# Optimization experiments

Measured on AMD Instinct MI355X. Metric: run time of the kernel, lower is better.

The kernel has to match this reference:

```python
import jax, jax.numpy as jnp
import numpy as np

B = 256        # batch size
D = 256        # feature dim
N = 100000     # memory bank size (num pseudo classes)
TEMP = 0.07    # SCT_Memory temperature


def setup_inputs() -> dict:
    key = jax.random.key(0)
    k1, k2, k3 = jax.random.split(key, 3)
    inputs = jax.random.normal(k1, (B, D), dtype=jnp.float32)
    # ReID features are L2-normalized before hitting the memory
    inputs = inputs / jnp.linalg.norm(inputs, axis=1, keepdims=True)
    indexes = jax.random.randint(k2, (B,), 0, N, dtype=jnp.int32)
    features = jax.random.normal(k3, (N, D), dtype=jnp.float32)
    features = features / jnp.linalg.norm(features, axis=1, keepdims=True)
    return {"inputs": inputs, "indexes": indexes, "features": features,
            "momentum": 0.2}


def reference(inputs, indexes, features, momentum):
    # ExemplarMemory.forward: outputs = inputs.mm(features.t())
    # SCT_Memory then scales by 1/temp to form cluster_score.
    out = jnp.matmul(inputs, features.T)  # [B, N]
    return out / TEMP
```

## Files before the change

### kernel.cpp

```cpp
#include <hip/hip_runtime.h>
#include <hip/hip_bf16.h>


typedef __attribute__((ext_vector_type(8))) __bf16 bf16x8;
typedef __attribute__((ext_vector_type(4))) float  floatx4;
typedef __attribute__((ext_vector_type(4))) unsigned int uint4v;

#define NB 100000
#define KD 256
#define BN 128
#define NTILES 782
#define GRID 256
#define NCHUNK 32

union FragCast { uint4v u; bf16x8 f; };

__device__ __forceinline__ unsigned pk(float a, float b) {
  __hip_bfloat162 h = __float22bfloat162_rn(float2{a, b});
  union { __hip_bfloat162 h2; unsigned u; } c; c.h2 = h; return c.u;
}

__device__ __forceinline__ void barrier_lgkm() {
  asm volatile("s_waitcnt lgkmcnt(0)" ::: "memory");
  __builtin_amdgcn_s_barrier();
  asm volatile("" ::: "memory");
}

__global__ __launch_bounds__(1024, 4)
void sct_gemm(const float* __restrict__ inputs,
              const float* __restrict__ features,
              float* __restrict__ out) {
  __shared__ uint4v lds[BN][NCHUNK];

  const int tid  = threadIdx.x;
  const int ws   = tid >> 6;
  const int lane = tid & 63;
  const int quad = lane >> 4;
  const int l16  = lane & 15;
  const int q4   = quad * 4;
  const int e3   = l16 & 7;

  const int b = blockIdx.x;
  const int ntiles = (NTILES - b + GRID - 1) / GRID;

  const int srow = tid >> 3, sk = tid & 7;
  const int rswz = srow & 7;

  float4 pf[8];
  {
    const int n0 = b * BN;
    #pragma unroll
    for (int j = 0; j < 8; ++j) pf[j] = make_float4(0.f, 0.f, 0.f, 0.f);
    if (n0 + srow < NB) {
      const float4* p = (const float4*)(features + (size_t)(n0 + srow) * KD + sk * 32);
      #pragma unroll
      for (int j = 0; j < 8; ++j) pf[j] = p[j];
    }
  }

  const float scale = 1.0f / 0.07f;
  bf16x8 afrag[8];
  {
    const float* arow = inputs + (ws * 16 + l16) * KD + quad * 8;
    #pragma unroll
    for (int t = 0; t < 8; ++t) {
      const float4* p = (const float4*)(arow + t * 32);
      const float4 a0 = p[0], a1 = p[1];
      FragCast fc;
      fc.u.x = pk(a0.x * scale, a0.y * scale);
      fc.u.y = pk(a0.z * scale, a0.w * scale);
      fc.u.z = pk(a1.x * scale, a1.y * scale);
      fc.u.w = pk(a1.z * scale, a1.w * scale);
      afrag[t] = fc.f;
    }
  }

  float* const orow = out + (size_t)(ws * 16 + l16) * NB;

  for (int it = 0; it < ntiles; ++it) {
    const int n0 = (b + it * GRID) * BN;

    barrier_lgkm();

    {
      #pragma unroll
      for (int j = 0; j < 4; ++j) {
        uint4v w;
        w.x = pk(pf[2 * j].x, pf[2 * j].y);
        w.y = pk(pf[2 * j].z, pf[2 * j].w);
        w.z = pk(pf[2 * j + 1].x, pf[2 * j + 1].y);
        w.w = pk(pf[2 * j + 1].z, pf[2 * j + 1].w);
        lds[srow][(sk * 4 + j) ^ rswz] = w;
      }
    }

    barrier_lgkm();

    if (it + 1 < ntiles) {
      const int nn0 = (b + (it + 1) * GRID) * BN;
      #pragma unroll
      for (int j = 0; j < 8; ++j) pf[j] = make_float4(0.f, 0.f, 0.f, 0.f);
      if (nn0 + srow < NB) {
        const float4* p = (const float4*)(features + (size_t)(nn0 + srow) * KD + sk * 32);
        #pragma unroll
        for (int j = 0; j < 8; ++j) pf[j] = p[j];
      }
    }

    floatx4 acc[8];
    #pragma unroll
    for (int nt = 0; nt < 8; ++nt) acc[nt] = floatx4{0.f, 0.f, 0.f, 0.f};

    #pragma unroll
    for (int t = 0; t < 8; ++t) {
      #pragma unroll
      for (int nt = 0; nt < 8; ++nt) {
        FragCast fc;
        fc.u = lds[nt * 16 + l16][(t * 4 + quad) ^ e3];
        acc[nt] = __builtin_amdgcn_mfma_f32_16x16x32_bf16(fc.f, afrag[t], acc[nt], 0, 0, 0);
      }
    }

    #pragma unroll
    for (int nt = 0; nt < 8; ++nt) {
      const int n = n0 + nt * 16 + q4;
      if (n < NB)
        *(floatx4*)(orow + n) = acc[nt];
    }
  }
}

extern "C" void kernel_launch(void* const* d_in, const int* in_sizes, int n_in,
                              void* d_out, int out_size, void* d_ws, size_t ws_size,
                              hipStream_t stream) {
  const float* inputs   = (const float*)d_in[0];
  const float* features = (const float*)d_in[2];
  float* out = (float*)d_out;

  sct_gemm<<<GRID, 1024, 0, stream>>>(inputs, features, out);
}
```

Baseline: 214.2 us.

## Split batch across blocks with smaller N tiles and more, smaller workgroups

Reorganizes the GEMM so each 256-thread block handles 64 batch rows and 32-column feature tiles, with four blocks sharing each feature tile group (1024 blocks total) instead of 256 blocks of 1024 threads covering all rows. The LDS layout switches from an XOR swizzle to a padded stride, bounds checks are dropped because 32 divides 100000 exactly, and s_setprio raises priority around the MFMA loop. This aims at better occupancy and latency hiding. In exchange each feature tile is loaded and converted four times, and each block does less work per barrier.

```diff
diff --git a/kernel.cpp b/kernel.cpp
--- a/kernel.cpp
+++ b/kernel.cpp
@@ -8,10 +8,12 @@
 
 #define NB 100000
 #define KD 256
-#define BN 128
-#define NTILES 782
-#define GRID 256
-#define NCHUNK 32
+#define BN 32
+#define NT32 3125
+#define NGROUPS 256
+#define GRID 1024
+#define BLK 256
+#define LDS_STRIDE 136
 
 union FragCast { uint4v u; bf16x8 f; };
 
@@ -26,11 +28,11 @@
   asm volatile("" ::: "memory");
 }
 
-__global__ __launch_bounds__(1024, 4)
+__global__ __launch_bounds__(BLK, 4)
 void sct_gemm(const float* __restrict__ inputs,
               const float* __restrict__ features,
               float* __restrict__ out) {
-  __shared__ uint4v lds[BN][NCHUNK];
+  __shared__ unsigned lds[BN * LDS_STRIDE];
 
   const int tid  = threadIdx.x;
   const int ws   = tid >> 6;
@@ -38,30 +40,26 @@
   const int quad = lane >> 4;
   const int l16  = lane & 15;
   const int q4   = quad * 4;
-  const int e3   = l16 & 7;
 
-  const int b = blockIdx.x;
-  const int ntiles = (NTILES - b + GRID - 1) / GRID;
+  const int b  = blockIdx.x;
+  const int g  = (b & 7) | ((b >> 5) << 3);
+  const int mh = (b >> 3) & 3;
+  const int ntiles = (NT32 - g + NGROUPS - 1) / NGROUPS;
 
   const int srow = tid >> 3, sk = tid & 7;
-  const int rswz = srow & 7;
 
   float4 pf[8];
   {
-    const int n0 = b * BN;
+    const int n0 = g * BN;
+    const float4* p = (const float4*)(features + (size_t)(n0 + srow) * KD + sk * 32);
     #pragma unroll
-    for (int j = 0; j < 8; ++j) pf[j] = make_float4(0.f, 0.f, 0.f, 0.f);
-    if (n0 + srow < NB) {
-      const float4* p = (const float4*)(features + (size_t)(n0 + srow) * KD + sk * 32);
-      #pragma unroll
-      for (int j = 0; j < 8; ++j) pf[j] = p[j];
-    }
+    for (int j = 0; j < 8; ++j) pf[j] = p[j];
   }
 
   const float scale = 1.0f / 0.07f;
   bf16x8 afrag[8];
   {
-    const float* arow = inputs + (ws * 16 + l16) * KD + quad * 8;
+    const float* arow = inputs + (mh * 64 + ws * 16 + l16) * KD + quad * 8;
     #pragma unroll
     for (int t = 0; t < 8; ++t) {
       const float4* p = (const float4*)(arow + t * 32);
@@ -75,10 +73,10 @@
     }
   }
 
-  float* const orow = out + (size_t)(ws * 16 + l16) * NB;
+  float* const orow = out + (size_t)(mh * 64 + ws * 16 + l16) * NB;
 
   for (int it = 0; it < ntiles; ++it) {
-    const int n0 = (b + it * GRID) * BN;
+    const int n0 = (g + it * NGROUPS) * BN;
 
     barrier_lgkm();
 
@@ -90,42 +88,39 @@
         w.y = pk(pf[2 * j].z, pf[2 * j].w);
         w.z = pk(pf[2 * j + 1].x, pf[2 * j + 1].y);
         w.w = pk(pf[2 * j + 1].z, pf[2 * j + 1].w);
-        lds[srow][(sk * 4 + j) ^ rswz] = w;
+        *(uint4v*)&lds[srow * LDS_STRIDE + (sk * 4 + j) * 4] = w;
       }
     }
 
     barrier_lgkm();
 
     if (it + 1 < ntiles) {
-      const int nn0 = (b + (it + 1) * GRID) * BN;
+      const int nn0 = (g + (it + 1) * NGROUPS) * BN;
+      const float4* p = (const float4*)(features + (size_t)(nn0 + srow) * KD + sk * 32);
       #pragma unroll
-      for (int j = 0; j < 8; ++j) pf[j] = make_float4(0.f, 0.f, 0.f, 0.f);
-      if (nn0 + srow < NB) {
-        const float4* p = (const float4*)(features + (size_t)(nn0 + srow) * KD + sk * 32);
-        #pragma unroll
-        for (int j = 0; j < 8; ++j) pf[j] = p[j];
-      }
+      for (int j = 0; j < 8; ++j) pf[j] = p[j];
     }
 
-    floatx4 acc[8];
+    floatx4 acc[2];
     #pragma unroll
-    for (int nt = 0; nt < 8; ++nt) acc[nt] = floatx4{0.f, 0.f, 0.f, 0.f};
+    for (int nt = 0; nt < 2; ++nt) acc[nt] = floatx4{0.f, 0.f, 0.f, 0.f};
 
+    __builtin_amdgcn_s_setprio(1);
     #pragma unroll
     for (int t = 0; t < 8; ++t) {
       #pragma unroll
-      for (int nt = 0; nt < 8; ++nt) {
+      for (int nt = 0; nt < 2; ++nt) {
         FragCast fc;
-        fc.u = lds[nt * 16 + l16][(t * 4 + quad) ^ e3];
+        fc.u = *(const uint4v*)&lds[(nt * 16 + l16) * LDS_STRIDE + t * 16 + q4];
         acc[nt] = __builtin_amdgcn_mfma_f32_16x16x32_bf16(fc.f, afrag[t], acc[nt], 0, 0, 0);
       }
     }
+    __builtin_amdgcn_s_setprio(0);
 
     #pragma unroll
-    for (int nt = 0; nt < 8; ++nt) {
+    for (int nt = 0; nt < 2; ++nt) {
       const int n = n0 + nt * 16 + q4;
-      if (n < NB)
-        *(floatx4*)(orow + n) = acc[nt];
+      *(floatx4*)(orow + n) = acc[nt];
     }
   }
 }
@@ -137,5 +132,5 @@
   const float* features = (const float*)d_in[2];
   float* out = (float*)d_out;
 
-  sct_gemm<<<GRID, 1024, 0, stream>>>(inputs, features, out);
+  sct_gemm<<<GRID, BLK, 0, stream>>>(inputs, features, out);
 }
```

Measured after the change: 233.6 us. 1.09x slower.
